# Kernel optimization log

Measured on AMD Instinct MI355X. Metric: run time of the kernel, lower is better.

## Reference

```python
import jax, jax.numpy as jnp
import numpy as np

B = 256            # number of graphs
N_NODES = 512      # nodes per graph
D = 128            # embedding_dim = hidden_dim
NUM_EDGE_CLASSES = 8
N_TOTAL = B * N_NODES
N_EDGES = N_TOTAL * 8   # avg degree 8
EDGES_DIM = N_NODES * (N_NODES - 1) // 2


def _ln(x, g, b):
    m = jnp.mean(x, axis=-1, keepdims=True)
    v = jnp.var(x, axis=-1, keepdims=True)
    return (x - m) * jax.lax.rsqrt(v + 1e-5) * g + b


def _mlp_ln(x, W1, b1, g, be, W2, b2):
    # MLP(input,hidden,output, n_hidden_layers=1, add_layer_norm=True):
    # Linear -> LayerNorm -> ReLU -> Linear
    return jax.nn.relu(_ln(x @ W1 + b1, g, be)) @ W2 + b2


def setup_inputs() -> dict:
    key = jax.random.key(0)
    ks = jax.random.split(key, 12)
    s = 1.0 / np.sqrt(D)
    return {
        "node_features": jax.random.randint(ks[0], (N_TOTAL, 1), 0, N_NODES),
        "edge_index": jax.random.randint(ks[1], (2, N_EDGES), 0, N_TOTAL),
        "batch_ptr": jnp.arange(B + 1, dtype=jnp.int32) * N_NODES,
        "emb": jax.random.normal(ks[2], (N_NODES, D), jnp.float32) * 0.02,
        "gin_W1": jax.random.normal(ks[3], (D, D), jnp.float32) * s,
        "gin_b1": jnp.zeros((D,), jnp.float32),
        "gin_g1": jnp.ones((D,), jnp.float32),
        "gin_be1": jnp.zeros((D,), jnp.float32),
        "gin_W2": jax.random.normal(ks[4], (D, D), jnp.float32) * s,
        "gin_b2": jnp.zeros((D,), jnp.float32),
        "post_W1": jax.random.normal(ks[5], (D, D), jnp.float32) * s,
        "post_b1": jnp.zeros((D,), jnp.float32),
        "post_W2": jax.random.normal(ks[6], (D, D), jnp.float32) * s,
        "post_b2": jnp.zeros((D,), jnp.float32),
        "norm_g": jnp.ones((D,), jnp.float32),
        "norm_b": jnp.zeros((D,), jnp.float32),
        "exit_W1": jax.random.normal(ks[7], (D, D), jnp.float32) * s,
        "exit_b1": jnp.zeros((D,), jnp.float32),
        "exit_g": jnp.ones((D,), jnp.float32),
        "exit_be": jnp.zeros((D,), jnp.float32),
        "exit_W2": jax.random.normal(ks[8], (D, 1), jnp.float32) * s,
        "exit_b2": jnp.zeros((1,), jnp.float32),
    }


def reference(node_features, edge_index, batch_ptr, emb,
              gin_W1, gin_b1, gin_g1, gin_be1, gin_W2, gin_b2,
              post_W1, post_b1, post_W2, post_b2,
              norm_g, norm_b,
              exit_W1, exit_b1, exit_g, exit_be, exit_W2, exit_b2):
    # node embedding lookup
    x = emb[node_features.squeeze(-1)]                      # [N_total, D]

    # single GIN conv layer (eps=0): MLP(x + sum_{j in N(i)} x_j)
    src, dst = edge_index[0], edge_index[1]
    agg = jax.ops.segment_sum(x[src], dst, num_segments=N_TOTAL)
    h = _mlp_ln(x + agg, gin_W1, gin_b1, gin_g1, gin_be1, gin_W2, gin_b2)
    # post-conv Sequential(Linear, ReLU, Linear)
    h = jax.nn.relu(h @ post_W1 + post_b1) @ post_W2 + post_b2
    # i == 0: no residual; then LayerNorm
    x = _ln(h, norm_g, norm_b)                              # [N_total, D]

    # segment mean via cumsum (faithful to _group_mean)
    cs = jnp.concatenate([jnp.zeros((1, D), x.dtype), jnp.cumsum(x, axis=0)], 0)
    sizes = (batch_ptr[1:] - batch_ptr[:-1]).astype(x.dtype)
    means = (cs[batch_ptr[1:]] - cs[batch_ptr[:-1]]) / sizes[:, None]  # [B, D]

    exit_action = _mlp_ln(means, exit_W1, exit_b1, exit_g, exit_be,
                          exit_W2, exit_b2).squeeze(-1)     # [B]

    # per-graph pairwise dot products, upper-triangular gather
    xb = x.reshape(B, N_NODES, D)
    scores = jnp.einsum('bnf,bmf->bnm', xb, xb) / jnp.sqrt(
        jnp.asarray(D, x.dtype))                            # [B, n, n]
    iu, ju = jnp.triu_indices(N_NODES, k=1)
    edge_actions = scores[:, iu, ju]                        # [B, EDGES_DIM]

    # action_type: index 1 = ADD_EDGE, 2 = EXIT (GraphActionType assumption)
    action_type = (jnp.zeros((B, 3), x.dtype)
                   .at[:, 1].set(1.0 - exit_action)
                   .at[:, 2].set(exit_action))
    edge_class = jnp.zeros((B, NUM_EDGE_CLASSES), x.dtype)
    node_class = jnp.zeros((B, 1), x.dtype)
    return (action_type, edge_class, node_class, edge_actions)
```

## Files before the change

kernel.cpp:

```cpp
#include <hip/hip_runtime.h>
#include <hip/hip_bf16.h>

#define NBATCH 256
#define NNODES 512
#define DIM    128
#define NTOT   (NBATCH*NNODES)
#define NEDGE  (NTOT*8)
#define EPB    130816
#define CAP    32

typedef __attribute__((ext_vector_type(8))) short  short8;
typedef __attribute__((ext_vector_type(4))) float  f32x4;

__device__ __forceinline__ unsigned short f2bf(float f){
  unsigned u = __builtin_bit_cast(unsigned, f);
  unsigned r = u + 0x7FFFu + ((u >> 16) & 1u);
  return (unsigned short)(r >> 16);
}

__global__ __launch_bounds__(256) void k_prep(
    const float* __restrict__ emb, const float* __restrict__ W1,
    unsigned short* __restrict__ embW1,
    const float* __restrict__ W2, const float* __restrict__ P1,
    const float* __restrict__ P2, unsigned short* __restrict__ wswz,
    int* __restrict__ cnt)
{
  const int tid = threadIdx.x;
  const int blk = blockIdx.x;
  __shared__ float er[2][DIM];
  if (blk < 256) {
    const int half = tid >> 7, c = tid & 127;
    const int r = blk*2 + half;
    er[half][c] = emb[r*DIM + c];
    __syncthreads();
    float acc = 0.f;
    #pragma unroll 8
    for (int k = 0; k < DIM; ++k) acc = fmaf(er[half][k], W1[k*DIM + c], acc);
    embW1[r*DIM + c] = f2bf(acc);
  } else if (blk < 448) {
    int idx = (blk - 256)*256 + tid;
    int s = idx >> 14, rem = idx & 16383;
    int ks = rem >> 12, n = (rem >> 9) & 7, lane = (rem >> 3) & 63, j = rem & 7;
    int lg = lane >> 4, l15 = lane & 15;
    int k = ks*32 + lg*8 + j, c = n*16 + l15;
    const float* src = (s == 0) ? W2 : ((s == 1) ? P1 : P2);
    wswz[idx] = f2bf(src[k*DIM + c]);
  } else {
    cnt[(blk - 448)*256 + tid] = 0;
  }
}

__global__ __launch_bounds__(256) void k_edges(const int* __restrict__ ei,
                                               const int* __restrict__ nf,
                                               int* __restrict__ cnt,
                                               unsigned short* __restrict__ slots){
  const int base = (blockIdx.x >> 3)*4096 + threadIdx.x;
  const int r    = blockIdx.x & 7;
  #pragma unroll
  for (int it = 0; it < 16; ++it) {
    const int e = base + it*256;
    const int d = ei[NEDGE + e];
    if ((d >> 14) == r) {
      const int s = ei[e];
      const int v = nf[s];
      const int pos = atomicAdd(&cnt[d], 1);
      if (pos < CAP) slots[(size_t)d*CAP + pos] = (unsigned short)v;
    }
  }
}

__global__ __launch_bounds__(1024, 1) void k_mega(
    const unsigned short* __restrict__ embW1, const int* __restrict__ nf,
    const int* __restrict__ cnt, const unsigned short* __restrict__ slots,
    const float* __restrict__ b1, const float* __restrict__ g1,
    const float* __restrict__ be1,
    const unsigned short* __restrict__ wswz,
    const float* __restrict__ b2,  const float* __restrict__ pb1, const float* __restrict__ pb2,
    const float* __restrict__ ng,  const float* __restrict__ nbv,
    const float* __restrict__ eW1, const float* __restrict__ eb1,
    const float* __restrict__ eg,  const float* __restrict__ ebe,
    const float* __restrict__ eW2, const float* __restrict__ eb2,
    float* __restrict__ out)
{
  __shared__ unsigned short X[512][136];
  __shared__ float gpart[16][128];
  __shared__ float mrow[128];
  __shared__ float redA[4];
  __shared__ float redB[2];
  const int tid   = threadIdx.x;
  const int bb    = blockIdx.x;
  const int nbase = bb * NNODES;

  {
    const int part = tid & 15;
    const short8* base8 = (const short8*)embW1;
    #pragma unroll 1
    for (int pass = 0; pass < 8; ++pass) {
      const int lnode = pass*64 + (tid >> 4);
      const int node  = nbase + lnode;
      const int self = nf[node];
      int m = cnt[node]; if (m > CAP) m = CAP;
      const unsigned short* sl = slots + (size_t)node*CAP;
      const uint4 sv0 = *(const uint4*)(sl);
      const uint4 sv1 = *(const uint4*)(sl + 8);
      const uint4 sv2 = *(const uint4*)(sl + 16);
      unsigned sw[12] = {sv0.x,sv0.y,sv0.z,sv0.w, sv1.x,sv1.y,sv1.z,sv1.w,
                         sv2.x,sv2.y,sv2.z,sv2.w};
      float a[8];
      {
        const float4* bp = (const float4*)(b1 + part*8);
        float4 x = bp[0], y = bp[1];
        a[0]=x.x; a[1]=x.y; a[2]=x.z; a[3]=x.w;
        a[4]=y.x; a[5]=y.y; a[6]=y.z; a[7]=y.w;
      }
#define ACC8(V) { _Pragma("unroll") \
      for (int i_ = 0; i_ < 8; ++i_) { \
        unsigned uu = ((unsigned)(unsigned short)(V)[i_]) << 16; \
        a[i_] += __builtin_bit_cast(float, uu); } }
      {
        short8 t0 = base8[(size_t)self*16 + part];
        short8 t[8];
        #pragma unroll
        for (int e = 0; e < 8; ++e) {
          unsigned id = (sw[e >> 1] >> ((e & 1)*16)) & 0xffffu;
          int idx = (e < m) ? (int)id : self;
          t[e] = base8[(size_t)idx*16 + part];
        }
        ACC8(t0)
        #pragma unroll
        for (int e = 0; e < 8; ++e) if (e < m) ACC8(t[e])
      }
      if (m > 8) {
        short8 t[8];
        #pragma unroll
        for (int e = 0; e < 8; ++e) {
          unsigned id = (sw[4 + (e >> 1)] >> ((e & 1)*16)) & 0xffffu;
          int idx = (e + 8 < m) ? (int)id : self;
          t[e] = base8[(size_t)idx*16 + part];
        }
        #pragma unroll
        for (int e = 0; e < 8; ++e) if (e + 8 < m) ACC8(t[e])
      }
      if (m > 16) {
        short8 t[8];
        #pragma unroll
        for (int e = 0; e < 8; ++e) {
          unsigned id = (sw[8 + (e >> 1)] >> ((e & 1)*16)) & 0xffffu;
          int idx = (e + 16 < m) ? (int)id : self;
          t[e] = base8[(size_t)idx*16 + part];
        }
        #pragma unroll
        for (int e = 0; e < 8; ++e) if (e + 16 < m) ACC8(t[e])
      }
      for (int e = 24; e < m; ++e) {
        short8 t = base8[(size_t)sl[e]*16 + part];
        ACC8(t)
      }
      float s = 0.f, qs = 0.f;
      #pragma unroll
      for (int i = 0; i < 8; ++i) { s += a[i]; qs += a[i]*a[i]; }
      #pragma unroll
      for (int msk = 1; msk < 16; msk <<= 1) {
        s  += __shfl_xor(s,  msk, 64);
        qs += __shfl_xor(qs, msk, 64);
      }
      const float mean = s * (1.f/128.f);
      const float var  = qs * (1.f/128.f) - mean*mean;
      const float rs   = rsqrtf(var + 1e-5f);
      const float4* gp = (const float4*)(g1  + part*8);
      const float4* ep = (const float4*)(be1 + part*8);
      float4 g0 = gp[0], g1v = gp[1], e0 = ep[0], e1v = ep[1];
      float gg[8] = {g0.x,g0.y,g0.z,g0.w, g1v.x,g1v.y,g1v.z,g1v.w};
      float eb[8] = {e0.x,e0.y,e0.z,e0.w, e1v.x,e1v.y,e1v.z,e1v.w};
      float v[8];
      #pragma unroll
      for (int i = 0; i < 8; ++i)
        v[i] = fmaxf((a[i] - mean)*rs*gg[i] + eb[i], 0.f);
      uint4 pk;
      pk.x = (unsigned)f2bf(v[0]) | ((unsigned)f2bf(v[1]) << 16);
      pk.y = (unsigned)f2bf(v[2]) | ((unsigned)f2bf(v[3]) << 16);
      pk.z = (unsigned)f2bf(v[4]) | ((unsigned)f2bf(v[5]) << 16);
      pk.w = (unsigned)f2bf(v[6]) | ((unsigned)f2bf(v[7]) << 16);
      *(uint4*)&X[lnode][part*8] = pk;
    }
  }
  __syncthreads();

  const int wave = tid >> 6, lane = tid & 63;
  const int l15 = lane & 15, lg = lane >> 4;
  const short8* ws8 = (const short8*)wswz;
  float pc[8];
  #pragma unroll
  for (int n = 0; n < 8; ++n) pc[n] = 0.f;

  #pragma unroll
  for (int s = 0; s < 3; ++s) {
    f32x4 acc[2][8];
    #pragma unroll
    for (int p2 = 0; p2 < 2; ++p2)
      #pragma unroll
      for (int n = 0; n < 8; ++n) acc[p2][n] = (f32x4){0.f,0.f,0.f,0.f};
    #pragma unroll
    for (int ks = 0; ks < 4; ++ks) {
      short8 bf[8];
      #pragma unroll
      for (int n = 0; n < 8; ++n) bf[n] = ws8[s*2048 + ks*512 + n*64 + lane];
      #pragma unroll
      for (int p2 = 0; p2 < 2; ++p2) {
        short8 af = *(const short8*)&X[p2*256 + wave*16 + l15][ks*32 + lg*8];
        #pragma unroll
        for (int n = 0; n < 8; ++n)
          acc[p2][n] = __builtin_amdgcn_mfma_f32_16x16x32_bf16(af, bf[n], acc[p2][n], 0, 0, 0);
      }
    }
    if (s < 2) {
      const float* bias = (s == 0) ? b2 : pb1;
      float bv[8];
      #pragma unroll
      for (int n = 0; n < 8; ++n) bv[n] = bias[n*16 + l15];
      #pragma unroll
      for (int p2 = 0; p2 < 2; ++p2)
        #pragma unroll
        for (int n = 0; n < 8; ++n)
          #pragma unroll
          for (int q = 0; q < 4; ++q) {
            float v = acc[p2][n][q] + bv[n];
            if (s == 1) v = fmaxf(v, 0.f);
            X[p2*256 + wave*16 + lg*4 + q][n*16 + l15] = f2bf(v);
          }
    } else {
      float bv[8], gc[8], bc[8];
      #pragma unroll
      for (int n = 0; n < 8; ++n) {
        bv[n] = pb2[n*16 + l15];
        gc[n] = ng [n*16 + l15];
        bc[n] = nbv[n*16 + l15];
      }
      #pragma unroll
      for (int p2 = 0; p2 < 2; ++p2) {
        float sr[4] = {0,0,0,0}, qr[4] = {0,0,0,0};
        #pragma unroll
        for (int n = 0; n < 8; ++n)
          #pragma unroll
          for (int q = 0; q < 4; ++q) {
            float v = acc[p2][n][q] + bv[n];
            acc[p2][n][q] = v;
            sr[q] += v; qr[q] += v*v;
          }
        #pragma unroll
        for (int msk = 1; msk < 16; msk <<= 1)
          #pragma unroll
          for (int q = 0; q < 4; ++q) {
            sr[q] += __shfl_xor(sr[q], msk, 64);
            qr[q] += __shfl_xor(qr[q], msk, 64);
          }
        float mean[4], rs[4];
        #pragma unroll
        for (int q = 0; q < 4; ++q) {
          mean[q] = sr[q]*(1.f/128.f);
          float var = qr[q]*(1.f/128.f) - mean[q]*mean[q];
          rs[q] = rsqrtf(var + 1e-5f);
        }
        #pragma unroll
        for (int n = 0; n < 8; ++n)
          #pragma unroll
          for (int q = 0; q < 4; ++q) {
            float xo = (acc[p2][n][q] - mean[q])*rs[q]*gc[n] + bc[n];
            X[p2*256 + wave*16 + lg*4 + q][n*16 + l15] = f2bf(xo);
            pc[n] += xo;
          }
      }
    }
  }
  #pragma unroll
  for (int n = 0; n < 8; ++n) {
    pc[n] += __shfl_xor(pc[n], 16, 64);
    pc[n] += __shfl_xor(pc[n], 32, 64);
  }
  if (lg == 0) {
    #pragma unroll
    for (int n = 0; n < 8; ++n) gpart[wave][n*16 + l15] = pc[n];
  }
  __syncthreads();

  if (tid < 128) {
    float m = 0.f;
    #pragma unroll
    for (int w = 0; w < 16; ++w) m += gpart[w][tid];
    mrow[tid] = m * (1.f/512.f);
  }
  __syncthreads();
  float uu = 0.f;
  if (tid < 128) {
    uu = eb1[tid];
    #pragma unroll 8
    for (int k = 0; k < DIM; ++k) uu = fmaf(mrow[k], eW1[k*DIM + tid], uu);
    float s2 = uu, q2 = uu*uu;
    #pragma unroll
    for (int msk = 1; msk < 64; msk <<= 1) {
      s2 += __shfl_xor(s2, msk, 64); q2 += __shfl_xor(q2, msk, 64);
    }
    if ((tid & 63) == 0) { redA[(tid >> 6)*2] = s2; redA[(tid >> 6)*2 + 1] = q2; }
  }
  __syncthreads();
  if (tid < 128) {
    const float S = redA[0] + redA[2], Q = redA[1] + redA[3];
    const float mean = S*(1.f/128.f);
    const float var  = Q*(1.f/128.f) - mean*mean;
    float av = fmaxf((uu - mean)*rsqrtf(var + 1e-5f)*eg[tid] + ebe[tid], 0.f);
    float p = av * eW2[tid];
    #pragma unroll
    for (int msk = 1; msk < 64; msk <<= 1) p += __shfl_xor(p, msk, 64);
    if ((tid & 63) == 0) redB[tid >> 6] = p;
  }
  __syncthreads();
  if (tid == 0) {
    float e = redB[0] + redB[1] + eb2[0];
    out[bb*3 + 0] = 0.f;
    out[bb*3 + 1] = 1.f - e;
    out[bb*3 + 2] = e;
  }
  if (tid < 8)   out[768 + bb*8 + tid] = 0.f;
  if (tid == 8)  out[2816 + bb] = 0.f;

  float* ea = out + 3072 + (size_t)bb*EPB;
  const float scale = 0.08838834764831845f;
  #pragma unroll 1
  for (int i = 0; i < 5; ++i) {
    const int task = wave*5 + i;
    const int p  = task >> 3, rg = task & 7;
    const int ti = (int)((0x3221110000ULL >> (p*4)) & 0xF);
    const int tj = (int)((0x3323213210ULL >> (p*4)) & 0xF);
    f32x4 acc[8];
    #pragma unroll
    for (int n = 0; n < 8; ++n) acc[n] = (f32x4){0,0,0,0};
    #pragma unroll
    for (int ks = 0; ks < 4; ++ks) {
      const int k0 = ks*32 + lg*8;
      short8 a0 = *(const short8*)&X[ti*128 + rg*16 + l15][k0];
      #pragma unroll
      for (int n = 0; n < 8; ++n) {
        short8 bf = *(const short8*)&X[tj*128 + n*16 + l15][k0];
        acc[n] = __builtin_amdgcn_mfma_f32_16x16x32_bf16(a0, bf, acc[n], 0, 0, 0);
      }
    }
    #pragma unroll
    for (int n = 0; n < 8; ++n) {
      const int gj = tj*128 + n*16 + l15;
      #pragma unroll
      for (int r = 0; r < 4; ++r) {
        const int gi = ti*128 + rg*16 + lg*4 + r;
        if (gi < gj) {
          const int rowbase = gi*511 - (gi*(gi-1))/2 - gi - 1;
          ea[rowbase + gj] = acc[n][r] * scale;
        }
      }
    }
  }
}

extern "C" void kernel_launch(void* const* d_in, const int* in_sizes, int n_in,
                              void* d_out, int out_size, void* d_ws, size_t ws_size,
                              hipStream_t stream) {
  const int*   nf   = (const int*)d_in[0];
  const int*   ei   = (const int*)d_in[1];
  const float* emb  = (const float*)d_in[3];
  const float* gW1  = (const float*)d_in[4];
  const float* gb1  = (const float*)d_in[5];
  const float* gg1  = (const float*)d_in[6];
  const float* gbe1 = (const float*)d_in[7];
  const float* gW2  = (const float*)d_in[8];
  const float* gb2  = (const float*)d_in[9];
  const float* pW1  = (const float*)d_in[10];
  const float* pb1  = (const float*)d_in[11];
  const float* pW2  = (const float*)d_in[12];
  const float* pb2  = (const float*)d_in[13];
  const float* ng   = (const float*)d_in[14];
  const float* nb   = (const float*)d_in[15];
  const float* eW1  = (const float*)d_in[16];
  const float* eb1  = (const float*)d_in[17];
  const float* eg   = (const float*)d_in[18];
  const float* ebe  = (const float*)d_in[19];
  const float* eW2  = (const float*)d_in[20];
  const float* eb2  = (const float*)d_in[21];
  float* out = (float*)d_out;

  char* ws = (char*)d_ws;
  unsigned short* embW1 = (unsigned short*)ws;
  unsigned short* wswz  = (unsigned short*)(ws + 262144);
  int*            cnt   = (int*)(ws + 360448);
  unsigned short* slots = (unsigned short*)(ws + 884736);
  if (ws_size < 9273344) return;

  k_prep  <<<960,  256, 0, stream>>>(emb, gW1, embW1, gW2, pW1, pW2, wswz, cnt);
  k_edges <<<2048, 256, 0, stream>>>(ei, nf, cnt, slots);
  k_mega  <<<256, 1024, 0, stream>>>(embW1, nf, cnt, slots, gb1, gg1, gbe1,
                                     wswz, gb2, pb1, pb2, ng, nb,
                                     eW1, eb1, eg, ebe, eW2, eb2, out);
}
```

Measured before the change: 146.2 us.

## Transpose pairwise MFMA output for row-contiguous float4 stores, skip lower tiles, dynamic tasks

The operands of the pairwise-score MFMA are swapped, so each lane holds four consecutive columns of one output row. Edge scores are then written as float4 stores along the packed upper-triangular row instead of scattered scalar stores. Diagonal tiles skip the MFMAs and stores for sub-diagonal 16-column blocks. Tasks come from an LDS atomic work queue rather than a fixed five per wave. The 1/sqrt(D) scale is folded in as D^-1/4 on X before bf16 rounding, and the exit MLP runs in one wave with fewer block barriers. Risks are the atomic overhead, slightly different bf16 rounding of X, and float4 stores that are only 4-byte aligned because of the triangular row offsets.

```diff
diff --git a/kernel.cpp b/kernel.cpp
--- a/kernel.cpp
+++ b/kernel.cpp
@@ -85,11 +85,11 @@
   __shared__ unsigned short X[512][136];
   __shared__ float gpart[16][128];
   __shared__ float mrow[128];
-  __shared__ float redA[4];
-  __shared__ float redB[2];
+  __shared__ int   tq;
   const int tid   = threadIdx.x;
   const int bb    = blockIdx.x;
   const int nbase = bb * NNODES;
+  if (tid == 0) tq = 0;
 
   {
     const int part = tid & 15;
@@ -189,6 +189,7 @@
   const int wave = tid >> 6, lane = tid & 63;
   const int l15 = lane & 15, lg = lane >> 4;
   const short8* ws8 = (const short8*)wswz;
+  const float PRESCL = 0.29730177875068026f;
   float pc[8];
   #pragma unroll
   for (int n = 0; n < 8; ++n) pc[n] = 0.f;
@@ -266,7 +267,7 @@
           #pragma unroll
           for (int q = 0; q < 4; ++q) {
             float xo = (acc[p2][n][q] - mean[q])*rs[q]*gc[n] + bc[n];
-            X[p2*256 + wave*16 + lg*4 + q][n*16 + l15] = f2bf(xo);
+            X[p2*256 + wave*16 + lg*4 + q][n*16 + l15] = f2bf(xo * PRESCL);
             pc[n] += xo;
           }
       }
@@ -283,77 +284,87 @@
   }
   __syncthreads();
 
-  if (tid < 128) {
-    float m = 0.f;
-    #pragma unroll
-    for (int w = 0; w < 16; ++w) m += gpart[w][tid];
-    mrow[tid] = m * (1.f/512.f);
-  }
-  __syncthreads();
-  float uu = 0.f;
-  if (tid < 128) {
-    uu = eb1[tid];
+  if (wave == 0) {
+    const int c0 = lane, c1 = lane + 64;
+    float m0 = 0.f, m1 = 0.f;
+    #pragma unroll
+    for (int w = 0; w < 16; ++w) { m0 += gpart[w][c0]; m1 += gpart[w][c1]; }
+    mrow[c0] = m0 * (1.f/512.f);
+    mrow[c1] = m1 * (1.f/512.f);
+    float u0 = eb1[c0], u1 = eb1[c1];
     #pragma unroll 8
-    for (int k = 0; k < DIM; ++k) uu = fmaf(mrow[k], eW1[k*DIM + tid], uu);
-    float s2 = uu, q2 = uu*uu;
+    for (int k = 0; k < DIM; ++k) {
+      const float mk = mrow[k];
+      u0 = fmaf(mk, eW1[k*DIM + c0], u0);
+      u1 = fmaf(mk, eW1[k*DIM + c1], u1);
+    }
+    float s2 = u0 + u1, q2 = u0*u0 + u1*u1;
     #pragma unroll
     for (int msk = 1; msk < 64; msk <<= 1) {
       s2 += __shfl_xor(s2, msk, 64); q2 += __shfl_xor(q2, msk, 64);
     }
-    if ((tid & 63) == 0) { redA[(tid >> 6)*2] = s2; redA[(tid >> 6)*2 + 1] = q2; }
-  }
-  __syncthreads();
-  if (tid < 128) {
-    const float S = redA[0] + redA[2], Q = redA[1] + redA[3];
-    const float mean = S*(1.f/128.f);
-    const float var  = Q*(1.f/128.f) - mean*mean;
-    float av = fmaxf((uu - mean)*rsqrtf(var + 1e-5f)*eg[tid] + ebe[tid], 0.f);
-    float p = av * eW2[tid];
+    const float mean = s2*(1.f/128.f);
+    const float var  = q2*(1.f/128.f) - mean*mean;
+    const float rs   = rsqrtf(var + 1e-5f);
+    float a0 = fmaxf((u0 - mean)*rs*eg[c0] + ebe[c0], 0.f);
+    float a1 = fmaxf((u1 - mean)*rs*eg[c1] + ebe[c1], 0.f);
+    float p = a0*eW2[c0] + a1*eW2[c1];
     #pragma unroll
     for (int msk = 1; msk < 64; msk <<= 1) p += __shfl_xor(p, msk, 64);
-    if ((tid & 63) == 0) redB[tid >> 6] = p;
-  }
-  __syncthreads();
-  if (tid == 0) {
-    float e = redB[0] + redB[1] + eb2[0];
-    out[bb*3 + 0] = 0.f;
-    out[bb*3 + 1] = 1.f - e;
-    out[bb*3 + 2] = e;
-  }
-  if (tid < 8)   out[768 + bb*8 + tid] = 0.f;
-  if (tid == 8)  out[2816 + bb] = 0.f;
+    if (lane == 0) {
+      float e = p + eb2[0];
+      out[bb*3 + 0] = 0.f;
+      out[bb*3 + 1] = 1.f - e;
+      out[bb*3 + 2] = e;
+    }
+  }
+  if (wave == 1) {
+    if (lane < 8)   out[768 + bb*8 + lane] = 0.f;
+    if (lane == 8)  out[2816 + bb] = 0.f;
+  }
 
   float* ea = out + 3072 + (size_t)bb*EPB;
-  const float scale = 0.08838834764831845f;
-  #pragma unroll 1
-  for (int i = 0; i < 5; ++i) {
-    const int task = wave*5 + i;
+  for (;;) {
+    int task = 0;
+    if (lane == 0) task = atomicAdd(&tq, 1);
+    task = __shfl(task, 0, 64);
+    if (task >= 80) break;
     const int p  = task >> 3, rg = task & 7;
     const int ti = (int)((0x3221110000ULL >> (p*4)) & 0xF);
     const int tj = (int)((0x3323213210ULL >> (p*4)) & 0xF);
+    const bool diag = (ti == tj);
+    const int nlo = diag ? rg : 0;
+
     f32x4 acc[8];
     #pragma unroll
     for (int n = 0; n < 8; ++n) acc[n] = (f32x4){0,0,0,0};
     #pragma unroll
     for (int ks = 0; ks < 4; ++ks) {
       const int k0 = ks*32 + lg*8;
-      short8 a0 = *(const short8*)&X[ti*128 + rg*16 + l15][k0];
+      short8 bfrag = *(const short8*)&X[ti*128 + rg*16 + l15][k0];
       #pragma unroll
       for (int n = 0; n < 8; ++n) {
-        short8 bf = *(const short8*)&X[tj*128 + n*16 + l15][k0];
-        acc[n] = __builtin_amdgcn_mfma_f32_16x16x32_bf16(a0, bf, acc[n], 0, 0, 0);
-      }
-    }
+        if (n >= nlo) {
+          short8 afrag = *(const short8*)&X[tj*128 + n*16 + l15][k0];
+          acc[n] = __builtin_amdgcn_mfma_f32_16x16x32_bf16(afrag, bfrag, acc[n], 0, 0, 0);
+        }
+      }
+    }
+    const int lgi = rg*16 + l15;
+    const int gi  = ti*128 + lgi;
+    const int rowbase = gi*511 - ((gi*(gi-1)) >> 1) - gi - 1;
+    float* rowp = ea + rowbase + tj*128;
     #pragma unroll
     for (int n = 0; n < 8; ++n) {
-      const int gj = tj*128 + n*16 + l15;
-      #pragma unroll
-      for (int r = 0; r < 4; ++r) {
-        const int gi = ti*128 + rg*16 + lg*4 + r;
-        if (gi < gj) {
-          const int rowbase = gi*511 - (gi*(gi-1))/2 - gi - 1;
-          ea[rowbase + gj] = acc[n][r] * scale;
-        }
+      if (n < nlo) continue;
+      const int lgj = n*16 + lg*4;
+      float4 v = make_float4(acc[n][0], acc[n][1], acc[n][2], acc[n][3]);
+      if (!diag || lgj > lgi) {
+        *(float4*)(rowp + lgj) = v;
+      } else if (lgj + 3 > lgi) {
+        #pragma unroll
+        for (int j = 1; j < 4; ++j)
+          if (lgj + j > lgi) rowp[lgj + j] = acc[n][j];
       }
     }
   }
```

After: 138.1 us. 5.6% less time.
